# Kernel tuning notes

Hardware: AMD Instinct MI355X
Metric: run time of the kernel (lower is better)

## Reference

```python
import jax, jax.numpy as jnp
import numpy as np

B, S, E, D, H = 4, 2048, 512, 64, 8
NEG = float(np.finfo(np.float64).min)  # tf uses tf.float64.min; overflows to -inf in fp32, same softmax effect


def setup_inputs() -> dict:
    key = jax.random.key(0)
    ks = jax.random.split(key, 6)
    std = 0.05  # tf.random_normal_initializer default stddev
    x = jax.random.normal(ks[0], (B, S, E), dtype=jnp.float32)
    Wq = jax.random.normal(ks[1], (H, E, D), dtype=jnp.float32) * std
    Wk = jax.random.normal(ks[2], (H, E, D), dtype=jnp.float32) * std
    Wvd = jax.random.normal(ks[3], (H, E, D), dtype=jnp.float32) * std
    Wvu = jax.random.normal(ks[4], (H, D, E), dtype=jnp.float32) * std
    Wo = jax.random.normal(ks[5], (H, 1), dtype=jnp.float32) * std
    return {"x": x, "Wq": Wq, "Wk": Wk, "Wvd": Wvd, "Wvu": Wvu, "Wo": Wo}


def reference(x, Wq, Wk, Wvd, Wvu, Wo):
    # Per-head projections, vectorized over the head axis h
    Q = jnp.einsum("bse,hed->bhsd", x, Wq)  # [B,H,S,D]
    K = jnp.einsum("bse,hed->bhsd", x, Wk)
    score = jnp.einsum("bhsd,bhtd->bhst", Q, K) / jnp.sqrt(jnp.float32(D))
    # tf.linalg.band_part(score, -1, 0): keep lower triangle (causal)
    tril = jnp.tril(jnp.ones((S, S), dtype=bool))
    score = jnp.where(tril, score, 0.0)
    # tf.where(score != 0, score, float64.min): masks zeros (incl. any exact-zero kept entries)
    score = jnp.where(score != 0, score, jnp.float32(NEG))
    attn = jax.nn.softmax(score, axis=-1)  # [B,H,S,S]
    # low-rank value projection: x @ (Wvdown @ Wvup) per head
    Wv = jnp.einsum("hed,hdf->hef", Wvd, Wvu)  # [H,E,E]
    V = jnp.einsum("bse,hef->bhsf", x, Wv)      # [B,H,S,E]
    heads = jnp.einsum("bhst,bhte->bhse", attn, V)  # [B,H,S,E]
    # stack on last axis then matmul with Wo[H,1] == weighted sum over heads
    out = jnp.einsum("bhse,h->bse", heads, Wo[:, 0])
    return out
```

## Files before the change

kernel.cpp:

```cpp
#include <hip/hip_runtime.h>
#include <math.h>
#include <type_traits>

namespace {
constexpr int B = 4, S = 2048, E = 512, D = 64, H = 8;
constexpr int KD = 512;

typedef short bf8 __attribute__((ext_vector_type(8)));
typedef short bf4 __attribute__((ext_vector_type(4)));
typedef float f4 __attribute__((ext_vector_type(4)));

__device__ __forceinline__ short f2bf(float f) {
  union { float f; unsigned u; } v; v.f = f;
  const unsigned r = v.u + 0x7fffu + ((v.u >> 16) & 1u);
  return (short)(r >> 16);
}

__device__ __forceinline__ unsigned cvt_pk_bf16(float a, float b) {
  unsigned r;
  asm("v_cvt_pk_bf16_f32 %0, %1, %2" : "=v"(r) : "v"(a), "v"(b));
  return r;
}

__device__ __forceinline__ void gload16(const void* g, void* l) {
  __builtin_amdgcn_global_load_lds(
      (const __attribute__((address_space(1))) unsigned int*)g,
      (__attribute__((address_space(3))) unsigned int*)l, 16, 0, 0);
}

__global__ __launch_bounds__(256) void prep_kernel(
    const float* __restrict__ x, const float* __restrict__ Wq,
    const float* __restrict__ Wk, const float* __restrict__ Wvd,
    const float* __restrict__ Wvu, const float* __restrict__ Wo,
    short* __restrict__ xb, short* __restrict__ WcatT,
    short* __restrict__ W2T) {
  __shared__ float T[64][65];
  const int bid = blockIdx.x;
  const int tid = threadIdx.x;
  if (bid < 2048) {
    const size_t i = ((size_t)bid * 256 + tid) * 8;
    const float4 v0 = *(const float4*)(x + i);
    const float4 v1 = *(const float4*)(x + i + 4);
    bf8 o;
    o[0] = f2bf(v0.x); o[1] = f2bf(v0.y); o[2] = f2bf(v0.z); o[3] = f2bf(v0.w);
    o[4] = f2bf(v1.x); o[5] = f2bf(v1.y); o[6] = f2bf(v1.z); o[7] = f2bf(v1.w);
    *(bf8*)(xb + i) = o;
  } else if (bid < 2240) {
    const int r = bid - 2048;
    const int cb = r >> 3, e0 = (r & 7) * 64;
    const int w = cb >> 3, h = cb & 7;
    const float* Wsel = (w == 0) ? Wq : (w == 1) ? Wk : Wvd;
    const float* Wp = Wsel + (size_t)h * E * D;
    const float qs = (cb < 8) ? 0.125f : 1.0f;
#pragma unroll
    for (int i = 0; i < 4; ++i) {
      const int f = tid + i * 256;
      const int rr = f >> 4, c4 = f & 15;
      const float4 v = *(const float4*)(Wp + (size_t)(e0 + rr) * D + c4 * 4);
      T[rr][c4 * 4 + 0] = v.x; T[rr][c4 * 4 + 1] = v.y;
      T[rr][c4 * 4 + 2] = v.z; T[rr][c4 * 4 + 3] = v.w;
    }
    __syncthreads();
#pragma unroll
    for (int i = 0; i < 4; ++i) {
      const int f = tid + i * 256;
      const int dr = f >> 4, e4 = f & 15;
      bf4 o;
#pragma unroll
      for (int j = 0; j < 4; ++j) o[j] = f2bf(T[e4 * 4 + j][dr] * qs);
      *(bf4*)(WcatT + (size_t)(cb * 64 + dr) * KD + e0 + e4 * 4) = o;
    }
  } else {
    const int r = bid - 2240;
    const int h = r >> 3, e0 = (r & 7) * 64;
    const float wo = Wo[h];
#pragma unroll
    for (int i = 0; i < 4; ++i) {
      const int f = tid + i * 256;
      const int rr = f >> 4, c4 = f & 15;
      const float4 v = *(const float4*)(Wvu + ((size_t)h * D + rr) * E + e0 + c4 * 4);
      T[rr][c4 * 4 + 0] = v.x * wo; T[rr][c4 * 4 + 1] = v.y * wo;
      T[rr][c4 * 4 + 2] = v.z * wo; T[rr][c4 * 4 + 3] = v.w * wo;
    }
    __syncthreads();
#pragma unroll
    for (int i = 0; i < 4; ++i) {
      const int f = tid + i * 256;
      const int er = f >> 4, d4 = f & 15;
      bf4 o;
#pragma unroll
      for (int j = 0; j < 4; ++j) o[j] = f2bf(T[d4 * 4 + j][er]);
      *(bf4*)(W2T + (size_t)(e0 + er) * KD + h * 64 + d4 * 4) = o;
    }
  }
}

template <int MODE>
__global__ __launch_bounds__(256) void gemm_kernel(
    const short* __restrict__ A, const short* __restrict__ Bt,
    short* __restrict__ Qb, short* __restrict__ Kb, short* __restrict__ Vtg,
    float* __restrict__ Of) {
  const int row0 = blockIdx.x * 128;
  const int ct = blockIdx.y;
  const int tid = threadIdx.x;
  const int w = tid >> 6, l = tid & 63;
  const int wm = w >> 1, wn = w & 1;
  const int lr = l & 15, hi = l >> 4;

  __shared__ short As[128 * 64];
  __shared__ short Bs[128 * 64];

  const short* Ag = A + (size_t)row0 * KD;
  const short* Bg = Bt + (size_t)ct * 128 * KD;

  f4 acc[4][4] = {};
  for (int k0 = 0; k0 < KD; k0 += 64) {
    __syncthreads();
#pragma unroll
    for (int i = 0; i < 4; ++i) {
      const int f = i * 256 + tid;
      const int r = f >> 3, g = f & 7;
      gload16(Ag + (size_t)r * KD + k0 + ((g ^ (r & 7)) << 3), &As[f * 8]);
    }
#pragma unroll
    for (int i = 0; i < 4; ++i) {
      const int f = i * 256 + tid;
      const int r = f >> 3, g = f & 7;
      gload16(Bg + (size_t)r * KD + k0 + ((g ^ (r & 7)) << 3), &Bs[f * 8]);
    }
    __syncthreads();

    bf8 af[4][2], bfv[4][2];
#pragma unroll
    for (int t = 0; t < 4; ++t) {
#pragma unroll
      for (int kh = 0; kh < 2; ++kh) {
        const int ar = wm * 64 + t * 16 + lr;
        af[t][kh] = *(const bf8*)&As[ar * 64 + (((kh * 4 + hi) ^ (ar & 7)) << 3)];
        const int br = wn * 64 + t * 16 + lr;
        bfv[t][kh] = *(const bf8*)&Bs[br * 64 + (((kh * 4 + hi) ^ (br & 7)) << 3)];
      }
    }
#pragma unroll
    for (int mt = 0; mt < 4; ++mt)
#pragma unroll
      for (int nt = 0; nt < 4; ++nt) {
        acc[mt][nt] =
            __builtin_amdgcn_mfma_f32_16x16x32_bf16(af[mt][0], bfv[nt][0], acc[mt][nt], 0, 0, 0);
        acc[mt][nt] =
            __builtin_amdgcn_mfma_f32_16x16x32_bf16(af[mt][1], bfv[nt][1], acc[mt][nt], 0, 0, 0);
      }
  }

  if constexpr (MODE == 0) {
#pragma unroll
    for (int nt = 0; nt < 4; ++nt) {
      const int gc = ct * 128 + wn * 64 + nt * 16 + lr;
      const int cb = gc >> 6, d = gc & 63;
      const int h = cb & 7;
      if (cb < 16) {
        short* Out = (cb < 8) ? Qb : Kb;
#pragma unroll
        for (int mt = 0; mt < 4; ++mt)
#pragma unroll
          for (int reg = 0; reg < 4; ++reg) {
            const int grow = row0 + wm * 64 + mt * 16 + hi * 4 + reg;
            const int b = grow >> 11, s = grow & (S - 1);
            Out[(((size_t)(b * H + h) * S + s) << 6) + d] = f2bf(acc[mt][nt][reg]);
          }
      } else {
        const int hswap = ((d >> 3) & 1) << 2;
#pragma unroll
        for (int mt = 0; mt < 4; ++mt) {
          const int grow0 = row0 + wm * 64 + mt * 16 + hi * 4;
          const int b = grow0 >> 11, s0 = (grow0 & (S - 1)) ^ hswap;
          bf4 o;
#pragma unroll
          for (int reg = 0; reg < 4; ++reg) o[reg] = f2bf(acc[mt][nt][reg]);
          *(bf4*)(Vtg + (((size_t)(b * H + h) * D + d) << 11) + s0) = o;
        }
      }
    }
  } else {
#pragma unroll
    for (int mt = 0; mt < 4; ++mt)
#pragma unroll
      for (int reg = 0; reg < 4; ++reg) {
        const int grow = row0 + wm * 64 + mt * 16 + hi * 4 + reg;
        float* orow = Of + (size_t)grow * 512 + ct * 128 + wn * 64;
#pragma unroll
        for (int nt = 0; nt < 4; ++nt) orow[nt * 16 + lr] = acc[mt][nt][reg];
      }
  }
}

__global__ __launch_bounds__(512, 4) void attn_kernel(
    const short* __restrict__ Qb, const short* __restrict__ Kb,
    const short* __restrict__ Vt, short* __restrict__ PVb) {
  const int bh = blockIdx.x;
  const int j = blockIdx.y;
  const int qtA = j, qtB = 31 - j;
  const int nA = j + 1, nB = 32 - j;
  const int sA = (nA + 1) >> 1;
  const int b = bh >> 3, h = bh & 7;
  const int tid = threadIdx.x;
  const int w = tid >> 6, l = tid & 63;
  const int wl = w & 3, g2 = w >> 2;
  const int lr = l & 15, hi = l >> 4;

  __shared__ short Ks[2][128 * 64];
  __shared__ short Vs[2][128 * 64];

  const short* QgA = Qb + ((size_t)bh * S + qtA * 64 + wl * 16 + lr) * D;
  const short* QgB = Qb + ((size_t)bh * S + qtB * 64 + wl * 16 + lr) * D;
  const bf8 qA0 = *(const bf8*)(QgA + hi * 8);
  const bf8 qA1 = *(const bf8*)(QgA + 32 + hi * 8);
  const bf8 qB0 = *(const bf8*)(QgB + hi * 8);
  const bf8 qB1 = *(const bf8*)(QgB + 32 + hi * 8);

  const short* Kg = Kb + (size_t)bh * S * D;
  const short* Vg = Vt + (size_t)bh * D * S;

  const int sr = tid >> 3, sg = tid & 7;
  const int sswz = (sg ^ (sr & 7)) << 3;
  const short* kg0 = Kg + (size_t)sr * D + sswz;
  const short* kg1 = Kg + (size_t)(sr + 64) * D + sswz;
  const short* vg0 = Vg + (size_t)sr * S + sswz;

  const int e7 = lr & 7;
  const int kla0 = lr * 128 + ((hi ^ e7) << 4);
  const int kla1 = kla0 ^ 64;
  const int x7 = (hi >> 1) ^ e7;
  const int swaph = ((hi & 1) ^ ((lr >> 3) & 1)) << 3;
  int vla[4];
#pragma unroll
  for (int np = 0; np < 4; ++np)
    vla[np] = lr * 128 + (((2 * np) ^ x7) << 4) + swaph;
  const int gofs = g2 * 8192;

  float lsA[4] = {}, lsB[4] = {};
  f4 accA[4] = {}, accB[4] = {};

  auto stage = [&](int snext, int bb) {
    const int kt0 = (snext < sA) ? 2 * snext : 2 * (snext - sA);
    const size_t ko = (size_t)kt0 << 12;
    const size_t vo = (size_t)kt0 << 6;
    gload16(kg0 + ko, &Ks[bb][tid * 8]);
    gload16(kg1 + ko, &Ks[bb][(512 + tid) * 8]);
    gload16(vg0 + vo, &Vs[bb][tid * 8]);
    gload16(vg0 + vo + 64, &Vs[bb][(512 + tid) * 8]);
  };

  auto step = [&](int bb, bf8 q0, bf8 q1, f4* aO, float* ls, auto diag_c) {
    constexpr bool DIAG = decltype(diag_c)::value;
    const char* Klb = (const char*)Ks[bb] + gofs;
    const char* Vlb = (const char*)Vs[bb] + gofs;
    f4 accS[4] = {};
    __builtin_amdgcn_s_setprio(1);
#pragma unroll
    for (int n = 0; n < 4; ++n) {
      const bf8 k0 = *(const bf8*)(Klb + kla0 + n * 2048);
      const bf8 k1 = *(const bf8*)(Klb + kla1 + n * 2048);
      accS[n] = __builtin_amdgcn_mfma_f32_16x16x32_bf16(k0, q0, accS[n], 0, 0, 0);
      accS[n] = __builtin_amdgcn_mfma_f32_16x16x32_bf16(k1, q1, accS[n], 0, 0, 0);
    }
    __builtin_amdgcn_s_setprio(0);

    bf4 pa[4];
#pragma unroll
    for (int n = 0; n < 4; ++n) {
      float p[4];
#pragma unroll
      for (int reg = 0; reg < 4; ++reg) {
        float pv = __expf(accS[n][reg]);
        if constexpr (DIAG) {
          const bool ok = (n * 16 + hi * 4 + reg) <= (wl * 16 + lr);
          pv = ok ? pv : 0.f;
        }
        p[reg] = pv;
        ls[reg] += pv;
      }
      union { int2 i; bf4 v; } u;
      u.i.x = (int)cvt_pk_bf16(p[0], p[1]);
      u.i.y = (int)cvt_pk_bf16(p[2], p[3]);
      pa[n] = u.v;
    }

    __builtin_amdgcn_s_setprio(1);
#pragma unroll
    for (int np = 0; np < 4; ++np) {
#pragma unroll
      for (int ne = 0; ne < 4; ++ne) {
        const bf4 vf = *(const bf4*)(Vlb + vla[np] + ne * 2048);
        aO[ne] = __builtin_amdgcn_mfma_f32_16x16x16bf16_1k(pa[np], vf, aO[ne], 0, 0, 0);
      }
    }
    __builtin_amdgcn_s_setprio(0);
  };

  auto epi = [&](int qt, f4* aO, float* ls) {
    float lv = (ls[0] + ls[1]) + (ls[2] + ls[3]);
    lv += __shfl_xor(lv, 16);
    lv += __shfl_xor(lv, 32);
#pragma unroll
    for (int reg = 0; reg < 4; ++reg) {
      const float lq = __shfl(lv, hi * 4 + reg);
      const float inv = 1.f / lq;
      const int s = qt * 64 + wl * 16 + hi * 4 + reg;
      short* op = PVb + (size_t)(b * S + s) * (H * D) + h * D;
#pragma unroll
      for (int n = 0; n < 4; ++n) op[n * 16 + lr] = f2bf(aO[n][reg] * inv);
    }
  };

  stage(0, 0);

  for (int s = 0; s < 17; ++s) {
    if (s > 0) {
      __builtin_amdgcn_s_barrier();
      __builtin_amdgcn_sched_barrier(0);
    }
    if (s < 16) {
      stage(s + 1, (s + 1) & 1);
      asm volatile("s_waitcnt vmcnt(4)" ::: "memory");
    } else {
      asm volatile("s_waitcnt vmcnt(0)" ::: "memory");
    }
    __builtin_amdgcn_sched_barrier(0);
    __builtin_amdgcn_s_barrier();
    __builtin_amdgcn_sched_barrier(0);

    const int bb = s & 1;
    if (s < sA) {
      const int c = 2 * s + g2;
      if (c < nA) {
        if (c == nA - 1) step(bb, qA0, qA1, accA, lsA, std::true_type{});
        else             step(bb, qA0, qA1, accA, lsA, std::false_type{});
      }
    } else {
      const int c = 2 * (s - sA) + g2;
      if (c < nB) {
        if (c == nB - 1) step(bb, qB0, qB1, accB, lsB, std::true_type{});
        else             step(bb, qB0, qB1, accB, lsB, std::false_type{});
      }
    }
  }

  __syncthreads();
  float* cbA = (float*)&Ks[0][0];
  float* cbB = (float*)&Vs[0][0];
  const int slot = (wl * 64 + l) * 20;
  if (g2 == 1) {
#pragma unroll
    for (int n = 0; n < 4; ++n)
#pragma unroll
      for (int reg = 0; reg < 4; ++reg) cbA[slot + n * 4 + reg] = accA[n][reg];
#pragma unroll
    for (int reg = 0; reg < 4; ++reg) cbA[slot + 16 + reg] = lsA[reg];
  } else {
#pragma unroll
    for (int n = 0; n < 4; ++n)
#pragma unroll
      for (int reg = 0; reg < 4; ++reg) cbB[slot + n * 4 + reg] = accB[n][reg];
#pragma unroll
    for (int reg = 0; reg < 4; ++reg) cbB[slot + 16 + reg] = lsB[reg];
  }
  __syncthreads();
  if (g2 == 0) {
#pragma unroll
    for (int n = 0; n < 4; ++n)
#pragma unroll
      for (int reg = 0; reg < 4; ++reg) accA[n][reg] += cbA[slot + n * 4 + reg];
#pragma unroll
    for (int reg = 0; reg < 4; ++reg) lsA[reg] += cbA[slot + 16 + reg];
    epi(qtA, accA, lsA);
  } else {
#pragma unroll
    for (int n = 0; n < 4; ++n)
#pragma unroll
      for (int reg = 0; reg < 4; ++reg) accB[n][reg] += cbB[slot + n * 4 + reg];
#pragma unroll
    for (int reg = 0; reg < 4; ++reg) lsB[reg] += cbB[slot + 16 + reg];
    epi(qtB, accB, lsB);
  }
}

}

extern "C" void kernel_launch(void* const* d_in, const int* in_sizes, int n_in,
                              void* d_out, int out_size, void* d_ws, size_t ws_size,
                              hipStream_t stream) {
  const float* x   = (const float*)d_in[0];
  const float* Wq  = (const float*)d_in[1];
  const float* Wk  = (const float*)d_in[2];
  const float* Wvd = (const float*)d_in[3];
  const float* Wvu = (const float*)d_in[4];
  const float* Wo  = (const float*)d_in[5];
  float* out = (float*)d_out;

  const size_t nqk = (size_t)B * H * S * D;
  short* xb    = (short*)d_ws;
  short* Qb    = xb + nqk;
  short* Kb    = Qb + nqk;
  short* Vtg   = Kb + nqk;
  short* PVb   = Vtg + nqk;
  short* WcatT = PVb + nqk;
  short* W2T   = WcatT + 1536 * KD;

  prep_kernel<<<dim3(2304), 256, 0, stream>>>(x, Wq, Wk, Wvd, Wvu, Wo,
                                              xb, WcatT, W2T);
  gemm_kernel<0><<<dim3(64, 12), 256, 0, stream>>>(xb, WcatT, Qb, Kb, Vtg, nullptr);
  attn_kernel<<<dim3(B * H, 16), 512, 0, stream>>>(Qb, Kb, Vtg, PVb);
  gemm_kernel<1><<<dim3(64, 4), 256, 0, stream>>>(PVb, W2T, nullptr, nullptr, nullptr, out);
}
```

Baseline: 75.30 us.

## Halve attention block to 256 threads with two query fragments per wave

Each attention wave now handles 32 query rows (two 16-row fragments) instead of 16. The block shrinks from 512 to 256 threads, and each thread issues twice as many K/V staging loads. Every K and V fragment read from LDS now feeds two MFMAs, which raises register reuse and cuts LDS traffic per FLOP. The cost is higher register pressure (doubled accumulators and score tiles) and fewer waves per block to hide latency, and the reduction buffer slot size doubles.

```diff
diff --git a/kernel.cpp b/kernel.cpp
--- a/kernel.cpp
+++ b/kernel.cpp
@@ -194,7 +194,7 @@
   }
 }
 
-__global__ __launch_bounds__(512, 4) void attn_kernel(
+__global__ __launch_bounds__(256) void attn_kernel(
     const short* __restrict__ Qb, const short* __restrict__ Kb,
     const short* __restrict__ Vt, short* __restrict__ PVb) {
   const int bh = blockIdx.x;
@@ -205,27 +205,38 @@
   const int b = bh >> 3, h = bh & 7;
   const int tid = threadIdx.x;
   const int w = tid >> 6, l = tid & 63;
-  const int wl = w & 3, g2 = w >> 2;
+  const int g2 = w >> 1, wl = w & 1;
   const int lr = l & 15, hi = l >> 4;
 
   __shared__ short Ks[2][128 * 64];
   __shared__ short Vs[2][128 * 64];
 
-  const short* QgA = Qb + ((size_t)bh * S + qtA * 64 + wl * 16 + lr) * D;
-  const short* QgB = Qb + ((size_t)bh * S + qtB * 64 + wl * 16 + lr) * D;
-  const bf8 qA0 = *(const bf8*)(QgA + hi * 8);
-  const bf8 qA1 = *(const bf8*)(QgA + 32 + hi * 8);
-  const bf8 qB0 = *(const bf8*)(QgB + hi * 8);
-  const bf8 qB1 = *(const bf8*)(QgB + 32 + hi * 8);
+  bf8 qA[2][2], qB[2][2];
+#pragma unroll
+  for (int f = 0; f < 2; ++f) {
+    const short* QgA =
+        Qb + ((size_t)bh * S + qtA * 64 + wl * 32 + f * 16 + lr) * D;
+    qA[f][0] = *(const bf8*)(QgA + hi * 8);
+    qA[f][1] = *(const bf8*)(QgA + 32 + hi * 8);
+    const short* QgB =
+        Qb + ((size_t)bh * S + qtB * 64 + wl * 32 + f * 16 + lr) * D;
+    qB[f][0] = *(const bf8*)(QgB + hi * 8);
+    qB[f][1] = *(const bf8*)(QgB + 32 + hi * 8);
+  }
 
   const short* Kg = Kb + (size_t)bh * S * D;
   const short* Vg = Vt + (size_t)bh * D * S;
 
-  const int sr = tid >> 3, sg = tid & 7;
-  const int sswz = (sg ^ (sr & 7)) << 3;
-  const short* kg0 = Kg + (size_t)sr * D + sswz;
-  const short* kg1 = Kg + (size_t)(sr + 64) * D + sswz;
-  const short* vg0 = Vg + (size_t)sr * S + sswz;
+  const int r0 = tid >> 3, fg = tid & 7;
+  const int sswz = (fg ^ (r0 & 7)) << 3;
+  const short* kp0 = Kg + (size_t)r0 * D + sswz;
+  const short* kp1 = Kg + (size_t)(r0 + 32) * D + sswz;
+  const short* kp2 = Kg + (size_t)(r0 + 64) * D + sswz;
+  const short* kp3 = Kg + (size_t)(r0 + 96) * D + sswz;
+  const short* vp0 = Vg + (size_t)r0 * S + sswz;
+  const short* vp1 = Vg + (size_t)(r0 + 32) * S + sswz;
+  const short* vp2 = vp0 + 64;
+  const short* vp3 = vp1 + 64;
 
   const int e7 = lr & 7;
   const int kla0 = lr * 128 + ((hi ^ e7) << 4);
@@ -238,52 +249,63 @@
     vla[np] = lr * 128 + (((2 * np) ^ x7) << 4) + swaph;
   const int gofs = g2 * 8192;
 
-  float lsA[4] = {}, lsB[4] = {};
-  f4 accA[4] = {}, accB[4] = {};
+  float lsA[2][4] = {}, lsB[2][4] = {};
+  f4 accA[2][4] = {}, accB[2][4] = {};
 
   auto stage = [&](int snext, int bb) {
     const int kt0 = (snext < sA) ? 2 * snext : 2 * (snext - sA);
     const size_t ko = (size_t)kt0 << 12;
     const size_t vo = (size_t)kt0 << 6;
-    gload16(kg0 + ko, &Ks[bb][tid * 8]);
-    gload16(kg1 + ko, &Ks[bb][(512 + tid) * 8]);
-    gload16(vg0 + vo, &Vs[bb][tid * 8]);
-    gload16(vg0 + vo + 64, &Vs[bb][(512 + tid) * 8]);
+    gload16(kp0 + ko, &Ks[bb][(0 * 256 + tid) * 8]);
+    gload16(kp1 + ko, &Ks[bb][(1 * 256 + tid) * 8]);
+    gload16(kp2 + ko, &Ks[bb][(2 * 256 + tid) * 8]);
+    gload16(kp3 + ko, &Ks[bb][(3 * 256 + tid) * 8]);
+    gload16(vp0 + vo, &Vs[bb][(0 * 256 + tid) * 8]);
+    gload16(vp1 + vo, &Vs[bb][(1 * 256 + tid) * 8]);
+    gload16(vp2 + vo, &Vs[bb][(2 * 256 + tid) * 8]);
+    gload16(vp3 + vo, &Vs[bb][(3 * 256 + tid) * 8]);
   };
 
-  auto step = [&](int bb, bf8 q0, bf8 q1, f4* aO, float* ls, auto diag_c) {
+  auto step = [&](int bb, bf8 (&q)[2][2], f4 (&aO)[2][4], float (&ls)[2][4],
+                  auto diag_c) {
     constexpr bool DIAG = decltype(diag_c)::value;
     const char* Klb = (const char*)Ks[bb] + gofs;
     const char* Vlb = (const char*)Vs[bb] + gofs;
-    f4 accS[4] = {};
+    f4 accS[2][4] = {};
     __builtin_amdgcn_s_setprio(1);
 #pragma unroll
     for (int n = 0; n < 4; ++n) {
       const bf8 k0 = *(const bf8*)(Klb + kla0 + n * 2048);
       const bf8 k1 = *(const bf8*)(Klb + kla1 + n * 2048);
-      accS[n] = __builtin_amdgcn_mfma_f32_16x16x32_bf16(k0, q0, accS[n], 0, 0, 0);
-      accS[n] = __builtin_amdgcn_mfma_f32_16x16x32_bf16(k1, q1, accS[n], 0, 0, 0);
+#pragma unroll
+      for (int f = 0; f < 2; ++f) {
+        accS[f][n] = __builtin_amdgcn_mfma_f32_16x16x32_bf16(k0, q[f][0], accS[f][n], 0, 0, 0);
+        accS[f][n] = __builtin_amdgcn_mfma_f32_16x16x32_bf16(k1, q[f][1], accS[f][n], 0, 0, 0);
+      }
     }
     __builtin_amdgcn_s_setprio(0);
 
-    bf4 pa[4];
-#pragma unroll
-    for (int n = 0; n < 4; ++n) {
-      float p[4];
-#pragma unroll
-      for (int reg = 0; reg < 4; ++reg) {
-        float pv = __expf(accS[n][reg]);
-        if constexpr (DIAG) {
-          const bool ok = (n * 16 + hi * 4 + reg) <= (wl * 16 + lr);
-          pv = ok ? pv : 0.f;
+    bf4 pa[2][4];
+#pragma unroll
+    for (int f = 0; f < 2; ++f) {
+#pragma unroll
+      for (int n = 0; n < 4; ++n) {
+        float p[4];
+#pragma unroll
+        for (int reg = 0; reg < 4; ++reg) {
+          float pv = __expf(accS[f][n][reg]);
+          if constexpr (DIAG) {
+            const bool ok = (n * 16 + hi * 4 + reg) <= (wl * 32 + f * 16 + lr);
+            pv = ok ? pv : 0.f;
+          }
+          p[reg] = pv;
+          ls[f][reg] += pv;
         }
-        p[reg] = pv;
-        ls[reg] += pv;
-      }
-      union { int2 i; bf4 v; } u;
-      u.i.x = (int)cvt_pk_bf16(p[0], p[1]);
-      u.i.y = (int)cvt_pk_bf16(p[2], p[3]);
-      pa[n] = u.v;
+        union { int2 i; bf4 v; } u;
+        u.i.x = (int)cvt_pk_bf16(p[0], p[1]);
+        u.i.y = (int)cvt_pk_bf16(p[2], p[3]);
+        pa[f][n] = u.v;
+      }
     }
 
     __builtin_amdgcn_s_setprio(1);
@@ -292,24 +314,28 @@
 #pragma unroll
       for (int ne = 0; ne < 4; ++ne) {
         const bf4 vf = *(const bf4*)(Vlb + vla[np] + ne * 2048);
-        aO[ne] = __builtin_amdgcn_mfma_f32_16x16x16bf16_1k(pa[np], vf, aO[ne], 0, 0, 0);
+        aO[0][ne] = __builtin_amdgcn_mfma_f32_16x16x16bf16_1k(pa[0][np], vf, aO[0][ne], 0, 0, 0);
+        aO[1][ne] = __builtin_amdgcn_mfma_f32_16x16x16bf16_1k(pa[1][np], vf, aO[1][ne], 0, 0, 0);
       }
     }
     __builtin_amdgcn_s_setprio(0);
   };
 
-  auto epi = [&](int qt, f4* aO, float* ls) {
-    float lv = (ls[0] + ls[1]) + (ls[2] + ls[3]);
-    lv += __shfl_xor(lv, 16);
-    lv += __shfl_xor(lv, 32);
-#pragma unroll
-    for (int reg = 0; reg < 4; ++reg) {
-      const float lq = __shfl(lv, hi * 4 + reg);
-      const float inv = 1.f / lq;
-      const int s = qt * 64 + wl * 16 + hi * 4 + reg;
-      short* op = PVb + (size_t)(b * S + s) * (H * D) + h * D;
-#pragma unroll
-      for (int n = 0; n < 4; ++n) op[n * 16 + lr] = f2bf(aO[n][reg] * inv);
+  auto epi = [&](int qt, f4 (&aO)[2][4], float (&ls)[2][4]) {
+#pragma unroll
+    for (int f = 0; f < 2; ++f) {
+      float lv = (ls[f][0] + ls[f][1]) + (ls[f][2] + ls[f][3]);
+      lv += __shfl_xor(lv, 16);
+      lv += __shfl_xor(lv, 32);
+#pragma unroll
+      for (int reg = 0; reg < 4; ++reg) {
+        const float lq = __shfl(lv, hi * 4 + reg);
+        const float inv = 1.f / lq;
+        const int srow = qt * 64 + wl * 32 + f * 16 + hi * 4 + reg;
+        short* op = PVb + (size_t)(b * S + srow) * (H * D) + h * D;
+#pragma unroll
+        for (int n = 0; n < 4; ++n) op[n * 16 + lr] = f2bf(aO[f][n][reg] * inv);
+      }
     }
   };
 
@@ -322,7 +348,7 @@
     }
     if (s < 16) {
       stage(s + 1, (s + 1) & 1);
-      asm volatile("s_waitcnt vmcnt(4)" ::: "memory");
+      asm volatile("s_waitcnt vmcnt(8)" ::: "memory");
     } else {
       asm volatile("s_waitcnt vmcnt(0)" ::: "memory");
     }
@@ -334,14 +360,14 @@
     if (s < sA) {
       const int c = 2 * s + g2;
       if (c < nA) {
-        if (c == nA - 1) step(bb, qA0, qA1, accA, lsA, std::true_type{});
-        else             step(bb, qA0, qA1, accA, lsA, std::false_type{});
+        if (c == nA - 1) step(bb, qA, accA, lsA, std::true_type{});
+        else             step(bb, qA, accA, lsA, std::false_type{});
       }
     } else {
       const int c = 2 * (s - sA) + g2;
       if (c < nB) {
-        if (c == nB - 1) step(bb, qB0, qB1, accB, lsB, std::true_type{});
-        else             step(bb, qB0, qB1, accB, lsB, std::false_type{});
+        if (c == nB - 1) step(bb, qB, accB, lsB, std::true_type{});
+        else             step(bb, qB, accB, lsB, std::false_type{});
       }
     }
   }
@@ -349,38 +375,58 @@
   __syncthreads();
   float* cbA = (float*)&Ks[0][0];
   float* cbB = (float*)&Vs[0][0];
-  const int slot = (wl * 64 + l) * 20;
+  const int slot = (wl * 64 + l) * 40;
   if (g2 == 1) {
 #pragma unroll
-    for (int n = 0; n < 4; ++n)
-#pragma unroll
-      for (int reg = 0; reg < 4; ++reg) cbA[slot + n * 4 + reg] = accA[n][reg];
-#pragma unroll
-    for (int reg = 0; reg < 4; ++reg) cbA[slot + 16 + reg] = lsA[reg];
+    for (int f = 0; f < 2; ++f) {
+#pragma unroll
+      for (int n = 0; n < 4; ++n)
+#pragma unroll
+        for (int reg = 0; reg < 4; ++reg)
+          cbA[slot + f * 20 + n * 4 + reg] = accA[f][n][reg];
+#pragma unroll
+      for (int reg = 0; reg < 4; ++reg)
+        cbA[slot + f * 20 + 16 + reg] = lsA[f][reg];
+    }
   } else {
 #pragma unroll
-    for (int n = 0; n < 4; ++n)
-#pragma unroll
-      for (int reg = 0; reg < 4; ++reg) cbB[slot + n * 4 + reg] = accB[n][reg];
-#pragma unroll
-    for (int reg = 0; reg < 4; ++reg) cbB[slot + 16 + reg] = lsB[reg];
+    for (int f = 0; f < 2; ++f) {
+#pragma unroll
+      for (int n = 0; n < 4; ++n)
+#pragma unroll
+        for (int reg = 0; reg < 4; ++reg)
+          cbB[slot + f * 20 + n * 4 + reg] = accB[f][n][reg];
+#pragma unroll
+      for (int reg = 0; reg < 4; ++reg)
+        cbB[slot + f * 20 + 16 + reg] = lsB[f][reg];
+    }
   }
   __syncthreads();
   if (g2 == 0) {
 #pragma unroll
-    for (int n = 0; n < 4; ++n)
-#pragma unroll
-      for (int reg = 0; reg < 4; ++reg) accA[n][reg] += cbA[slot + n * 4 + reg];
-#pragma unroll
-    for (int reg = 0; reg < 4; ++reg) lsA[reg] += cbA[slot + 16 + reg];
+    for (int f = 0; f < 2; ++f) {
+#pragma unroll
+      for (int n = 0; n < 4; ++n)
+#pragma unroll
+        for (int reg = 0; reg < 4; ++reg)
+          accA[f][n][reg] += cbA[slot + f * 20 + n * 4 + reg];
+#pragma unroll
+      for (int reg = 0; reg < 4; ++reg)
+        lsA[f][reg] += cbA[slot + f * 20 + 16 + reg];
+    }
     epi(qtA, accA, lsA);
   } else {
 #pragma unroll
-    for (int n = 0; n < 4; ++n)
-#pragma unroll
-      for (int reg = 0; reg < 4; ++reg) accB[n][reg] += cbB[slot + n * 4 + reg];
-#pragma unroll
-    for (int reg = 0; reg < 4; ++reg) lsB[reg] += cbB[slot + 16 + reg];
+    for (int f = 0; f < 2; ++f) {
+#pragma unroll
+      for (int n = 0; n < 4; ++n)
+#pragma unroll
+        for (int reg = 0; reg < 4; ++reg)
+          accB[f][n][reg] += cbB[slot + f * 20 + n * 4 + reg];
+#pragma unroll
+      for (int reg = 0; reg < 4; ++reg)
+        lsB[f][reg] += cbB[slot + f * 20 + 16 + reg];
+    }
     epi(qtB, accB, lsB);
   }
 }
@@ -410,6 +456,6 @@
   prep_kernel<<<dim3(2304), 256, 0, stream>>>(x, Wq, Wk, Wvd, Wvu, Wo,
                                               xb, WcatT, W2T);
   gemm_kernel<0><<<dim3(64, 12), 256, 0, stream>>>(xb, WcatT, Qb, Kb, Vtg, nullptr);
-  attn_kernel<<<dim3(B * H, 16), 512, 0, stream>>>(Qb, Kb, Vtg, PVb);
+  attn_kernel<<<dim3(B * H, 16), 256, 0, stream>>>(Qb, Kb, Vtg, PVb);
   gemm_kernel<1><<<dim3(64, 4), 256, 0, stream>>>(PVb, W2T, nullptr, nullptr, nullptr, out);
 }
```

After: 80.01 us. 6.2% more time.
